# Kernel optimization log

Hardware: AMD Instinct MI355X
Metric: run time of the kernel (lower is better)

## Reference

```python
import jax, jax.numpy as jnp
import numpy as np


def setup_inputs() -> dict:
    key = jax.random.key(0)
    ks = jax.random.split(key, 12)
    b, S, c, d = 2, 20, 256, 4
    sc = 0.05

    def w(k, shape):
        return jax.random.normal(k, shape, jnp.float32) * sc

    return {
        "x": jax.random.normal(ks[0], (b, S, c, d, d), jnp.float32),
        "W1": w(ks[1], (2 * (c + 2), 256)), "b1": jnp.zeros((256,), jnp.float32),
        "W2": w(ks[2], (256, 256)), "b2": jnp.zeros((256,), jnp.float32),
        "W3": w(ks[3], (256, 256)), "b3": jnp.zeros((256,), jnp.float32),
        "W4": w(ks[4], (256, 256)), "b4": jnp.zeros((256,), jnp.float32),
        "Wf1": w(ks[5], (256, 256)), "bf1": jnp.zeros((256,), jnp.float32),
        "Wf2": w(ks[6], (256, 256)), "bf2": jnp.zeros((256,), jnp.float32),
        "Wf3": w(ks[7], (256, 29)), "bf3": jnp.zeros((29,), jnp.float32),
        "Wf4": w(ks[8], (29, 1)), "bf4": jnp.zeros((1,), jnp.float32),
    }


def reference(x, W1, b1, W2, b2, W3, b3, W4, b4,
              Wf1, bf1, Wf2, bf2, Wf3, bf3, Wf4, bf4):
    # x: [b, S, c, d, d] post-repnet features
    b, S, c, d, _ = x.shape
    cc = c + 2  # feature channels after coord concat
    # coord[0,i,j] = i/d, coord[1,i,j] = j/d (matches torch transpose chain)
    r = jnp.arange(d, dtype=x.dtype) / d
    coord = jnp.stack(jnp.meshgrid(r, r, indexing="ij"), axis=0)  # [2, d, d]
    xc = jnp.concatenate(
        [x, jnp.broadcast_to(coord, (b, S, 2, d, d))], axis=2)     # [b,S,cc,d,d]
    xf = xc.reshape(b, S, cc, d * d).transpose(0, 1, 3, 2)         # [b,S,P,cc]

    # First g layer on concat([x_i, x_j]) == split W1 and broadcast-add.
    # Pair feature at (b, s1, s2, p1, p2) = [x[b,s2,:,p2], x[b,s1,:,p1]].
    A = jnp.einsum("bspc,ch->bsph", xf, W1[:cc])   # x_i contribution
    B = jnp.einsum("bspc,ch->bsph", xf, W1[cc:])   # x_j contribution
    h = jax.nn.relu(A[:, None, :, None, :, :] + B[:, :, None, :, None, :] + b1)
    # h: [b, S, S, P, P, 256]
    h = jax.nn.relu(h @ W2 + b2)
    h = jax.nn.relu(h @ W3 + b3)
    h = jax.nn.relu(h @ W4 + b4)
    pooled = h.sum(axis=(3, 4))                    # [b, S, S, 256]

    y = jax.nn.relu(pooled @ Wf1 + bf1)
    y = jax.nn.relu(y @ Wf2 + bf2)  # Dropout is identity in eval/reference
    y = jax.nn.relu(y @ Wf3 + bf3)
    score = jax.nn.sigmoid(y @ Wf4 + bf4)[..., 0]  # [b, S, S]
    return score
```

## Files before the change

### kernel.cpp

```cpp
#include <hip/hip_runtime.h>
#include <hip/hip_bf16.h>
#include <math.h>

typedef _Float16 f16x8 __attribute__((ext_vector_type(8)));
typedef _Float16 f16x4 __attribute__((ext_vector_type(4)));
typedef float f32x4 __attribute__((ext_vector_type(4)));

#define LDH 264

__global__ void prep_ab(const float* __restrict__ x, const float* __restrict__ W1,
                        const float* __restrict__ b1,
                        float* __restrict__ A, float* __restrict__ B) {
    int blk = blockIdx.x;
    int bs = blk >> 2, pg = blk & 3;
    __shared__ float xs[258 * 4];
    for (int i = threadIdx.x; i < 1024; i += 512) {
        int c = i >> 2, pp = i & 3;
        xs[i] = x[bs * 4096 + c * 16 + pg * 4 + pp];
    }
    if (threadIdx.x < 8) {
        int pp = threadIdx.x & 3, c = 256 + (threadIdx.x >> 2);
        int p = pg * 4 + pp;
        xs[c * 4 + pp] = (float)((c == 256) ? (p >> 2) : (p & 3)) * 0.25f;
    }
    __syncthreads();
    int half = threadIdx.x >> 8;
    int col  = threadIdx.x & 255;
    float acc[4] = {0.f, 0.f, 0.f, 0.f};
    const float* Wp = W1 + half * 258 * 256 + col;
    for (int c = 0; c < 258; c++) {
        float w = Wp[c * 256];
#pragma unroll
        for (int pp = 0; pp < 4; pp++) acc[pp] += xs[c * 4 + pp] * w;
    }
    float* out = half ? B : A;
    float bias = half ? 0.f : b1[col];
#pragma unroll
    for (int pp = 0; pp < 4; pp++)
        out[(bs * 16 + pg * 4 + pp) * 256 + col] = acc[pp] + bias;
}

__global__ void prep_w(const float* __restrict__ W2, const float* __restrict__ W3,
                       const float* __restrict__ W4, _Float16* __restrict__ Wt) {
    int blk = blockIdx.x;
    int t   = threadIdx.x;
    int kk = blk & 7, cg = (blk >> 3) & 15, L = blk >> 7;
    int l = t >> 3, e = t & 7;
    int col = cg * 16 + (l & 15);
    int k   = kk * 32 + (l >> 4) * 8 + e;
    const float* W = (L == 0) ? W2 : (L == 1) ? W3 : W4;
    Wt[blk * 512 + t] = (_Float16)W[k * 256 + col];
}

__global__ __launch_bounds__(512, 4) void pairnet(
        const float* __restrict__ A, const float* __restrict__ B,
        const _Float16* __restrict__ Wt,
        const float* __restrict__ b2, const float* __restrict__ b3,
        const float* __restrict__ b4, float* __restrict__ pooled4) {
    __shared__ _Float16 hb[128 * LDH];

    int blk  = blockIdx.x;
    int half = blk & 1;
    int bss  = blk >> 1;
    int s2   = bss % 20;
    int s1   = (bss / 20) % 20;
    int b    = bss / 400;
    int tid  = threadIdx.x;

    const float* Abase = A + (b * 20 + s2) * 16 * 256;
    const float* Bbase = B + ((b * 20 + s1) * 16 + half * 8) * 256;
#pragma unroll
    for (int it = 0; it < 8; it++) {
        int u = it * 512 + tid;
        int r = u >> 5;
        int c = (u & 31) * 8;
        const float* Ap = Abase + (r & 15) * 256 + c;
        const float* Bp = Bbase + (r >> 4) * 256 + c;
        float4 a0 = *(const float4*)(Ap);
        float4 a1 = *(const float4*)(Ap + 4);
        float4 b0 = *(const float4*)(Bp);
        float4 b1 = *(const float4*)(Bp + 4);
        f16x8 hv;
        hv[0] = (_Float16)fmaxf(a0.x + b0.x, 0.f);
        hv[1] = (_Float16)fmaxf(a0.y + b0.y, 0.f);
        hv[2] = (_Float16)fmaxf(a0.z + b0.z, 0.f);
        hv[3] = (_Float16)fmaxf(a0.w + b0.w, 0.f);
        hv[4] = (_Float16)fmaxf(a1.x + b1.x, 0.f);
        hv[5] = (_Float16)fmaxf(a1.y + b1.y, 0.f);
        hv[6] = (_Float16)fmaxf(a1.z + b1.z, 0.f);
        hv[7] = (_Float16)fmaxf(a1.w + b1.w, 0.f);
        *(f16x8*)(hb + r * LDH + c) = hv;
    }
    __syncthreads();

    int wid = tid >> 6, lane = tid & 63;
    int row0 = (wid >> 2) * 64;
    int col0 = (wid & 3) * 64;
    int lr = lane & 15, lk = lane >> 4;

#pragma unroll
    for (int L = 0; L < 3; L++) {
        const float* bias = (L == 0) ? b2 : (L == 1) ? b3 : b4;
        const _Float16* wb = Wt + (size_t)((L * 16 + (wid & 3) * 4) * 8) * 512 + lane * 8;

        f32x4 acc[4][4];
#pragma unroll
        for (int m = 0; m < 4; m++)
#pragma unroll
            for (int n = 0; n < 4; n++) acc[m][n] = (f32x4){0.f, 0.f, 0.f, 0.f};

#pragma unroll
        for (int kk = 0; kk < 8; kk++) {
            f16x8 w[4], a[4];
#pragma unroll
            for (int n = 0; n < 4; n++)
                w[n] = *(const f16x8*)(wb + (n * 8 + kk) * 512);
#pragma unroll
            for (int m = 0; m < 4; m++)
                a[m] = *(const f16x8*)(hb + (row0 + 16 * m + lr) * LDH + kk * 32 + 8 * lk);
#pragma unroll
            for (int m = 0; m < 4; m++)
#pragma unroll
                for (int n = 0; n < 4; n++)
                    acc[m][n] = __builtin_amdgcn_mfma_f32_16x16x32_f16(
                        w[n], a[m], acc[m][n], 0, 0, 0);
        }

        if (L < 2) {
            __syncthreads();
#pragma unroll
            for (int n = 0; n < 4; n++) {
                int cb = col0 + 16 * n + 4 * lk;
                float4 b4v = *(const float4*)(bias + cb);
#pragma unroll
                for (int m = 0; m < 4; m++) {
                    int row = row0 + 16 * m + lr;
                    f16x4 hv;
                    hv[0] = (_Float16)fmaxf(acc[m][n][0] + b4v.x, 0.f);
                    hv[1] = (_Float16)fmaxf(acc[m][n][1] + b4v.y, 0.f);
                    hv[2] = (_Float16)fmaxf(acc[m][n][2] + b4v.z, 0.f);
                    hv[3] = (_Float16)fmaxf(acc[m][n][3] + b4v.w, 0.f);
                    *(f16x4*)(hb + row * LDH + cb) = hv;
                }
            }
            __syncthreads();
        } else {
#pragma unroll
            for (int n = 0; n < 4; n++) {
                int cb = col0 + 16 * n + 4 * lk;
                float4 b4v = *(const float4*)(bias + cb);
                f32x4 s = (f32x4){0.f, 0.f, 0.f, 0.f};
#pragma unroll
                for (int m = 0; m < 4; m++) {
                    s[0] += fmaxf(acc[m][n][0] + b4v.x, 0.f);
                    s[1] += fmaxf(acc[m][n][1] + b4v.y, 0.f);
                    s[2] += fmaxf(acc[m][n][2] + b4v.z, 0.f);
                    s[3] += fmaxf(acc[m][n][3] + b4v.w, 0.f);
                }
#pragma unroll
                for (int mask = 1; mask <= 8; mask <<= 1) {
#pragma unroll
                    for (int c = 0; c < 4; c++) s[c] += __shfl_xor(s[c], mask);
                }
                if (lr == 0) {
                    int slab = half * 2 + (wid >> 2);
                    float4 sv; sv.x = s[0]; sv.y = s[1]; sv.z = s[2]; sv.w = s[3];
                    *(float4*)(pooled4 + ((size_t)slab * 800 + bss) * 256 + cb) = sv;
                }
            }
        }
    }
}

__global__ void final_mlp(const float* __restrict__ pooled4,
        const float* __restrict__ Wf1, const float* __restrict__ bf1,
        const float* __restrict__ Wf2, const float* __restrict__ bf2,
        const float* __restrict__ Wf3, const float* __restrict__ bf3,
        const float* __restrict__ Wf4, const float* __restrict__ bf4,
        float* __restrict__ out) {
    __shared__ float p[4][256], y[4][256], z[4][256], y3[4][29];
    int r0 = blockIdx.x * 4;
    int t  = threadIdx.x;
    for (int i = t; i < 1024; i += 256) {
        int r = i >> 8, c = i & 255;
        float v = 0.f;
#pragma unroll
        for (int q = 0; q < 4; q++)
            v += pooled4[((size_t)q * 800 + r0 + r) * 256 + c];
        p[r][c] = v;
    }
    __syncthreads();
    float acc[4];
#pragma unroll
    for (int r = 0; r < 4; r++) acc[r] = bf1[t];
    for (int k = 0; k < 256; k++) {
        float w = Wf1[k * 256 + t];
#pragma unroll
        for (int r = 0; r < 4; r++) acc[r] += p[r][k] * w;
    }
#pragma unroll
    for (int r = 0; r < 4; r++) y[r][t] = fmaxf(acc[r], 0.f);
    __syncthreads();
#pragma unroll
    for (int r = 0; r < 4; r++) acc[r] = bf2[t];
    for (int k = 0; k < 256; k++) {
        float w = Wf2[k * 256 + t];
#pragma unroll
        for (int r = 0; r < 4; r++) acc[r] += y[r][k] * w;
    }
#pragma unroll
    for (int r = 0; r < 4; r++) z[r][t] = fmaxf(acc[r], 0.f);
    __syncthreads();
    if (t < 116) {
        int r = t / 29, c = t % 29;
        float a = bf3[c];
        for (int k = 0; k < 256; k++) a += z[r][k] * Wf3[k * 29 + c];
        y3[r][c] = fmaxf(a, 0.f);
    }
    __syncthreads();
    if (t < 4) {
        float zz = bf4[0];
#pragma unroll
        for (int c = 0; c < 29; c++) zz += y3[t][c] * Wf4[c];
        out[r0 + t] = 1.f / (1.f + expf(-zz));
    }
}

extern "C" void kernel_launch(void* const* d_in, const int* in_sizes, int n_in,
                              void* d_out, int out_size, void* d_ws, size_t ws_size,
                              hipStream_t stream) {
    const float* x   = (const float*)d_in[0];
    const float* W1  = (const float*)d_in[1];
    const float* b1  = (const float*)d_in[2];
    const float* W2  = (const float*)d_in[3];
    const float* b2  = (const float*)d_in[4];
    const float* W3  = (const float*)d_in[5];
    const float* b3  = (const float*)d_in[6];
    const float* W4  = (const float*)d_in[7];
    const float* b4  = (const float*)d_in[8];
    const float* Wf1 = (const float*)d_in[9];
    const float* bf1 = (const float*)d_in[10];
    const float* Wf2 = (const float*)d_in[11];
    const float* bf2 = (const float*)d_in[12];
    const float* Wf3 = (const float*)d_in[13];
    const float* bf3 = (const float*)d_in[14];
    const float* Wf4 = (const float*)d_in[15];
    const float* bf4 = (const float*)d_in[16];

    float* A       = (float*)d_ws;
    float* B       = A + 640 * 256;
    float* pooled4 = B + 640 * 256;
    _Float16* Wt   = (_Float16*)(pooled4 + 4 * 800 * 256);

    prep_ab<<<160, 512, 0, stream>>>(x, W1, b1, A, B);
    prep_w<<<384, 512, 0, stream>>>(W2, W3, W4, Wt);
    pairnet<<<1600, 512, 0, stream>>>(A, B, Wt, b2, b3, b4, pooled4);
    final_mlp<<<200, 256, 0, stream>>>(pooled4, Wf1, bf1, Wf2, bf2, Wf3, bf3, Wf4, bf4,
                                       (float*)d_out);
}
```

Measured before the change: 124.6 us.

## Switch pairnet to 32x32x16 MFMA with register prefetch and merge prep kernels

```diff
diff --git a/kernel.cpp b/kernel.cpp
--- a/kernel.cpp
+++ b/kernel.cpp
@@ -5,15 +5,29 @@
 typedef _Float16 f16x8 __attribute__((ext_vector_type(8)));
 typedef _Float16 f16x4 __attribute__((ext_vector_type(4)));
 typedef float f32x4 __attribute__((ext_vector_type(4)));
+typedef float f32x16 __attribute__((ext_vector_type(16)));
 
 #define LDH 264
 
-__global__ void prep_ab(const float* __restrict__ x, const float* __restrict__ W1,
-                        const float* __restrict__ b1,
-                        float* __restrict__ A, float* __restrict__ B) {
-    int blk = blockIdx.x;
+__global__ void prep(const float* __restrict__ x, const float* __restrict__ W1,
+                     const float* __restrict__ b1,
+                     const float* __restrict__ W2, const float* __restrict__ W3,
+                     const float* __restrict__ W4,
+                     float* __restrict__ A, float* __restrict__ B,
+                     _Float16* __restrict__ Wt) {
+    __shared__ float xs[258 * 4];
+    if (blockIdx.x < 384) {
+        int blk = blockIdx.x, t = threadIdx.x;
+        int ks = blk & 15, cg = (blk >> 4) & 7, L = blk >> 7;
+        int l = t >> 3, e = t & 7;
+        int col = cg * 32 + (l & 31);
+        int k   = ks * 16 + (l >> 5) * 8 + e;
+        const float* W = (L == 0) ? W2 : (L == 1) ? W3 : W4;
+        Wt[blk * 512 + t] = (_Float16)W[k * 256 + col];
+        return;
+    }
+    int blk = blockIdx.x - 384;
     int bs = blk >> 2, pg = blk & 3;
-    __shared__ float xs[258 * 4];
     for (int i = threadIdx.x; i < 1024; i += 512) {
         int c = i >> 2, pp = i & 3;
         xs[i] = x[bs * 4096 + c * 16 + pg * 4 + pp];
@@ -38,18 +52,6 @@
 #pragma unroll
     for (int pp = 0; pp < 4; pp++)
         out[(bs * 16 + pg * 4 + pp) * 256 + col] = acc[pp] + bias;
-}
-
-__global__ void prep_w(const float* __restrict__ W2, const float* __restrict__ W3,
-                       const float* __restrict__ W4, _Float16* __restrict__ Wt) {
-    int blk = blockIdx.x;
-    int t   = threadIdx.x;
-    int kk = blk & 7, cg = (blk >> 3) & 15, L = blk >> 7;
-    int l = t >> 3, e = t & 7;
-    int col = cg * 16 + (l & 15);
-    int k   = kk * 32 + (l >> 4) * 8 + e;
-    const float* W = (L == 0) ? W2 : (L == 1) ? W3 : W4;
-    Wt[blk * 512 + t] = (_Float16)W[k * 256 + col];
 }
 
 __global__ __launch_bounds__(512, 4) void pairnet(
@@ -91,81 +93,101 @@
         hv[7] = (_Float16)fmaxf(a1.w + b1.w, 0.f);
         *(f16x8*)(hb + r * LDH + c) = hv;
     }
-    __syncthreads();
 
     int wid = tid >> 6, lane = tid & 63;
     int row0 = (wid >> 2) * 64;
+    int cg0  = (wid & 3) * 2;
     int col0 = (wid & 3) * 64;
-    int lr = lane & 15, lk = lane >> 4;
+    int l31 = lane & 31, hi = lane >> 5;
+
+    const _Float16* abase = hb + (row0 + l31) * LDH + hi * 8;
+
+    const _Float16* wb0 = Wt + (size_t)(cg0 * 16) * 512 + lane * 8;
+    f16x8 pw0 = *(const f16x8*)(wb0);
+    f16x8 pw1 = *(const f16x8*)(wb0 + 16 * 512);
+    __syncthreads();
 
 #pragma unroll
     for (int L = 0; L < 3; L++) {
         const float* bias = (L == 0) ? b2 : (L == 1) ? b3 : b4;
-        const _Float16* wb = Wt + (size_t)((L * 16 + (wid & 3) * 4) * 8) * 512 + lane * 8;
-
-        f32x4 acc[4][4];
-#pragma unroll
-        for (int m = 0; m < 4; m++)
-#pragma unroll
-            for (int n = 0; n < 4; n++) acc[m][n] = (f32x4){0.f, 0.f, 0.f, 0.f};
-
-#pragma unroll
-        for (int kk = 0; kk < 8; kk++) {
-            f16x8 w[4], a[4];
-#pragma unroll
-            for (int n = 0; n < 4; n++)
-                w[n] = *(const f16x8*)(wb + (n * 8 + kk) * 512);
-#pragma unroll
-            for (int m = 0; m < 4; m++)
-                a[m] = *(const f16x8*)(hb + (row0 + 16 * m + lr) * LDH + kk * 32 + 8 * lk);
-#pragma unroll
-            for (int m = 0; m < 4; m++)
-#pragma unroll
-                for (int n = 0; n < 4; n++)
-                    acc[m][n] = __builtin_amdgcn_mfma_f32_16x16x32_f16(
-                        w[n], a[m], acc[m][n], 0, 0, 0);
+        const _Float16* wL = Wt + (size_t)((L * 8 + cg0) * 16) * 512 + lane * 8;
+
+        f32x16 acc00{}, acc01{}, acc10{}, acc11{};
+        f16x8 cw0 = pw0, cw1 = pw1;
+        f16x8 ca0 = *(const f16x8*)(abase);
+        f16x8 ca1 = *(const f16x8*)(abase + 32 * LDH);
+#pragma unroll
+        for (int ks = 0; ks < 16; ks++) {
+            f16x8 nw0, nw1, na0, na1;
+            if (ks < 15) {
+                nw0 = *(const f16x8*)(wL + (ks + 1) * 512);
+                nw1 = *(const f16x8*)(wL + (16 + ks + 1) * 512);
+                na0 = *(const f16x8*)(abase + (ks + 1) * 16);
+                na1 = *(const f16x8*)(abase + 32 * LDH + (ks + 1) * 16);
+            }
+            acc00 = __builtin_amdgcn_mfma_f32_32x32x16_f16(cw0, ca0, acc00, 0, 0, 0);
+            acc01 = __builtin_amdgcn_mfma_f32_32x32x16_f16(cw1, ca0, acc01, 0, 0, 0);
+            acc10 = __builtin_amdgcn_mfma_f32_32x32x16_f16(cw0, ca1, acc10, 0, 0, 0);
+            acc11 = __builtin_amdgcn_mfma_f32_32x32x16_f16(cw1, ca1, acc11, 0, 0, 0);
+            cw0 = nw0; cw1 = nw1; ca0 = na0; ca1 = na1;
         }
 
         if (L < 2) {
             __syncthreads();
-#pragma unroll
-            for (int n = 0; n < 4; n++) {
-                int cb = col0 + 16 * n + 4 * lk;
-                float4 b4v = *(const float4*)(bias + cb);
-#pragma unroll
-                for (int m = 0; m < 4; m++) {
-                    int row = row0 + 16 * m + lr;
-                    f16x4 hv;
-                    hv[0] = (_Float16)fmaxf(acc[m][n][0] + b4v.x, 0.f);
-                    hv[1] = (_Float16)fmaxf(acc[m][n][1] + b4v.y, 0.f);
-                    hv[2] = (_Float16)fmaxf(acc[m][n][2] + b4v.z, 0.f);
-                    hv[3] = (_Float16)fmaxf(acc[m][n][3] + b4v.w, 0.f);
-                    *(f16x4*)(hb + row * LDH + cb) = hv;
+            const _Float16* wN = Wt + (size_t)(((L + 1) * 8 + cg0) * 16) * 512 + lane * 8;
+            pw0 = *(const f16x8*)(wN);
+            pw1 = *(const f16x8*)(wN + 16 * 512);
+#pragma unroll
+            for (int ni = 0; ni < 2; ni++) {
+                const f32x16& aN0 = ni ? acc01 : acc00;
+                const f32x16& aN1 = ni ? acc11 : acc10;
+#pragma unroll
+                for (int q = 0; q < 4; q++) {
+                    int cb = col0 + 32 * ni + 8 * q + 4 * hi;
+                    float4 bv = *(const float4*)(bias + cb);
+                    f16x4 h0, h1;
+                    h0[0] = (_Float16)fmaxf(aN0[4 * q + 0] + bv.x, 0.f);
+                    h0[1] = (_Float16)fmaxf(aN0[4 * q + 1] + bv.y, 0.f);
+                    h0[2] = (_Float16)fmaxf(aN0[4 * q + 2] + bv.z, 0.f);
+                    h0[3] = (_Float16)fmaxf(aN0[4 * q + 3] + bv.w, 0.f);
+                    h1[0] = (_Float16)fmaxf(aN1[4 * q + 0] + bv.x, 0.f);
+                    h1[1] = (_Float16)fmaxf(aN1[4 * q + 1] + bv.y, 0.f);
+                    h1[2] = (_Float16)fmaxf(aN1[4 * q + 2] + bv.z, 0.f);
+                    h1[3] = (_Float16)fmaxf(aN1[4 * q + 3] + bv.w, 0.f);
+                    *(f16x4*)(hb + (row0 + l31) * LDH + cb) = h0;
+                    *(f16x4*)(hb + (row0 + 32 + l31) * LDH + cb) = h1;
                 }
             }
             __syncthreads();
         } else {
 #pragma unroll
-            for (int n = 0; n < 4; n++) {
-                int cb = col0 + 16 * n + 4 * lk;
-                float4 b4v = *(const float4*)(bias + cb);
-                f32x4 s = (f32x4){0.f, 0.f, 0.f, 0.f};
-#pragma unroll
-                for (int m = 0; m < 4; m++) {
-                    s[0] += fmaxf(acc[m][n][0] + b4v.x, 0.f);
-                    s[1] += fmaxf(acc[m][n][1] + b4v.y, 0.f);
-                    s[2] += fmaxf(acc[m][n][2] + b4v.z, 0.f);
-                    s[3] += fmaxf(acc[m][n][3] + b4v.w, 0.f);
+            for (int ni = 0; ni < 2; ni++) {
+                const f32x16& aN0 = ni ? acc01 : acc00;
+                const f32x16& aN1 = ni ? acc11 : acc10;
+                float s[16];
+#pragma unroll
+                for (int q = 0; q < 4; q++) {
+                    int cb = col0 + 32 * ni + 8 * q + 4 * hi;
+                    float4 bv = *(const float4*)(bias + cb);
+                    s[4 * q + 0] = fmaxf(aN0[4 * q + 0] + bv.x, 0.f) + fmaxf(aN1[4 * q + 0] + bv.x, 0.f);
+                    s[4 * q + 1] = fmaxf(aN0[4 * q + 1] + bv.y, 0.f) + fmaxf(aN1[4 * q + 1] + bv.y, 0.f);
+                    s[4 * q + 2] = fmaxf(aN0[4 * q + 2] + bv.z, 0.f) + fmaxf(aN1[4 * q + 2] + bv.z, 0.f);
+                    s[4 * q + 3] = fmaxf(aN0[4 * q + 3] + bv.w, 0.f) + fmaxf(aN1[4 * q + 3] + bv.w, 0.f);
                 }
 #pragma unroll
-                for (int mask = 1; mask <= 8; mask <<= 1) {
-#pragma unroll
-                    for (int c = 0; c < 4; c++) s[c] += __shfl_xor(s[c], mask);
-                }
-                if (lr == 0) {
+                for (int mask = 1; mask <= 16; mask <<= 1)
+#pragma unroll
+                    for (int r = 0; r < 16; r++) s[r] += __shfl_xor(s[r], mask);
+                if (l31 == 0) {
                     int slab = half * 2 + (wid >> 2);
-                    float4 sv; sv.x = s[0]; sv.y = s[1]; sv.z = s[2]; sv.w = s[3];
-                    *(float4*)(pooled4 + ((size_t)slab * 800 + bss) * 256 + cb) = sv;
+                    float* pp = pooled4 + ((size_t)slab * 800 + bss) * 256;
+#pragma unroll
+                    for (int q = 0; q < 4; q++) {
+                        float4 sv;
+                        sv.x = s[4 * q + 0]; sv.y = s[4 * q + 1];
+                        sv.z = s[4 * q + 2]; sv.w = s[4 * q + 3];
+                        *(float4*)(pp + col0 + 32 * ni + 8 * q + 4 * hi) = sv;
+                    }
                 }
             }
         }
@@ -252,8 +274,7 @@
     float* pooled4 = B + 640 * 256;
     _Float16* Wt   = (_Float16*)(pooled4 + 4 * 800 * 256);
 
-    prep_ab<<<160, 512, 0, stream>>>(x, W1, b1, A, B);
-    prep_w<<<384, 512, 0, stream>>>(W2, W3, W4, Wt);
+    prep<<<544, 512, 0, stream>>>(x, W1, b1, W2, W3, W4, A, B, Wt);
     pairnet<<<1600, 512, 0, stream>>>(A, B, Wt, b2, b3, b4, pooled4);
     final_mlp<<<200, 256, 0, stream>>>(pooled4, Wf1, bf1, Wf2, bf2, Wf3, bf3, Wf4, bf4,
                                        (float*)d_out);
```

After: 139.8 us. 1.12x slower.
